# Optimization experiments

Hardware: AMD Instinct MI355X
Metric: run time of the kernel (lower is better)

The kernel has to match this reference:

```python
import jax, jax.numpy as jnp
import numpy as np

DELTA = 0.1  # init kwarg delta
EPS = 1e-12


def setup_inputs() -> dict:
    key = jax.random.key(0)
    k1, k2 = jax.random.split(key)
    N = 16384  # flattened element count; pairwise matrix is N x N (1 GB fp32)
    logits = jax.random.normal(k1, (N,), dtype=jnp.float32)
    targets = jax.random.randint(k2, (N,), 0, 2, dtype=jnp.int32)
    pos_weight = jnp.float32(1.0)  # registered buffer (non-trainable)
    return {"logits": logits, "targets": targets, "pos_weight": pos_weight}


def reference(logits, targets, pos_weight):
    y = targets.reshape(-1).astype(logits.dtype)
    x = logits.reshape(-1)
    pred = jax.nn.sigmoid(x)
    # g uses pred.detach() in torch -> stop_gradient here
    g = jnp.abs(jax.lax.stop_gradient(pred) - y)  # [N]
    n = g.shape[0]
    # brute-force O(n^2) gradient-density estimate (torch.no_grad block)
    diff = jnp.abs(g[:, None] - g[None, :])            # [N, N]
    GD = jnp.sum((diff <= DELTA).astype(g.dtype), axis=1) / DELTA  # [N]
    beta = jax.lax.stop_gradient(n / (GD + EPS))       # [N]
    # binary_cross_entropy_with_logits with pos_weight, reduction='none':
    # pw * y * softplus(-x) + (1 - y) * softplus(x)
    per_elem = pos_weight * y * jax.nn.softplus(-x) + (1.0 - y) * jax.nn.softplus(x)
    weighted = jnp.mean(beta * per_elem)
    pure_mean = jnp.mean(per_elem)
    return weighted, pure_mean
```

## Files before the change

kernel.cpp:

```cpp
#include <hip/hip_runtime.h>
#include <math.h>

#define GHM_DELTA 0.1f
#define GHM_EPS   1e-12f

__device__ __forceinline__ float softplus_ref(float x) {
    return fmaxf(x, 0.0f) + log1pf(expf(-fabsf(x)));
}

__device__ __forceinline__ float sigmoid_ref(float x) {
    return 1.0f / (1.0f + expf(-x));
}

__global__ __launch_bounds__(512) void ghm_fused(
    const float* __restrict__ logits,
    const int*   __restrict__ targets,
    const float* __restrict__ pos_weight,
    double*      __restrict__ partials,
    int n)
{
    __shared__ float gj[16384];
    __shared__ int   pc[16][32];

    const int tid = threadIdx.x;
    const int bx  = blockIdx.x;

    {
        const float4* l4 = reinterpret_cast<const float4*>(logits);
        const int4*   t4 = reinterpret_cast<const int4*>(targets);
        float4*       g4 = reinterpret_cast<float4*>(gj);
        const int nf4 = n >> 2;
        for (int k = tid; k < nf4; k += 512) {
            float4 x = l4[k];
            int4   y = t4[k];
            float4 r;
            r.x = fabsf(sigmoid_ref(x.x) - (float)y.x);
            r.y = fabsf(sigmoid_ref(x.y) - (float)y.y);
            r.z = fabsf(sigmoid_ref(x.z) - (float)y.z);
            r.w = fabsf(sigmoid_ref(x.w) - (float)y.w);
            g4[k] = r;
        }
    }
    __syncthreads();

    const int ilane = tid & 31;
    const int jpart = tid >> 5;
    const int ig    = bx * 32 + ilane;
    const float gi  = gj[ig];

    int c0 = 0, c1 = 0, c2 = 0, c3 = 0;
    const float4* lj = reinterpret_cast<const float4*>(gj) + jpart * 256;
    #pragma unroll 8
    for (int jj = 0; jj < 256; ++jj) {
        float4 v = lj[jj];
        c0 += (fabsf(gi - v.x) <= GHM_DELTA) ? 1 : 0;
        c1 += (fabsf(gi - v.y) <= GHM_DELTA) ? 1 : 0;
        c2 += (fabsf(gi - v.z) <= GHM_DELTA) ? 1 : 0;
        c3 += (fabsf(gi - v.w) <= GHM_DELTA) ? 1 : 0;
    }
    pc[jpart][ilane] = (c0 + c1) + (c2 + c3);
    __syncthreads();

    if (tid < 64) {
        double wd = 0.0, pd = 0.0;
        if (tid < 32) {
            int cnt = 0;
            #pragma unroll
            for (int p = 0; p < 16; ++p) cnt += pc[p][tid];
            const int i = bx * 32 + tid;
            float x  = logits[i];
            float y  = (float)targets[i];
            float GD   = (float)cnt / GHM_DELTA;
            float beta = (float)n / (GD + GHM_EPS);
            float pw   = pos_weight[0];
            float per  = pw * y * softplus_ref(-x) + (1.0f - y) * softplus_ref(x);
            wd = (double)(beta * per);
            pd = (double)per;
        }
        #pragma unroll
        for (int off = 32; off >= 1; off >>= 1) {
            wd += __shfl_down(wd, off, 64);
            pd += __shfl_down(pd, off, 64);
        }
        if (tid == 0) {
            partials[bx * 2]     = wd;
            partials[bx * 2 + 1] = pd;
        }
    }
}

__global__ __launch_bounds__(512) void ghm_reduce(
    const double* __restrict__ partials,
    float* __restrict__ out,
    int nb, int n)
{
    __shared__ double red[16];
    const int t = threadIdx.x;
    double wd = 0.0, pd = 0.0;
    for (int k = t; k < nb; k += 512) {
        wd += partials[2 * k];
        pd += partials[2 * k + 1];
    }
    #pragma unroll
    for (int off = 32; off >= 1; off >>= 1) {
        wd += __shfl_down(wd, off, 64);
        pd += __shfl_down(pd, off, 64);
    }
    const int wave = t >> 6;
    if ((t & 63) == 0) { red[wave * 2] = wd; red[wave * 2 + 1] = pd; }
    __syncthreads();
    if (t == 0) {
        double sw = 0.0, sp = 0.0;
        for (int k = 0; k < 8; ++k) { sw += red[2 * k]; sp += red[2 * k + 1]; }
        out[0] = (float)(sw / (double)n);
        out[1] = (float)(sp / (double)n);
    }
}

extern "C" void kernel_launch(void* const* d_in, const int* in_sizes, int n_in,
                              void* d_out, int out_size, void* d_ws, size_t ws_size,
                              hipStream_t stream) {
    const float* logits     = (const float*)d_in[0];
    const int*   targets    = (const int*)d_in[1];
    const float* pos_weight = (const float*)d_in[2];
    float* out = (float*)d_out;
    const int n = in_sizes[0];

    const int nb = n / 32;
    double* partials = (double*)d_ws;

    ghm_fused<<<nb, 512, 0, stream>>>(logits, targets, pos_weight, partials, n);
    ghm_reduce<<<1, 512, 0, stream>>>(partials, out, nb, n);
}
```

Before: 37.78 us.

## Register-block 8 rows per thread and widen blocks to 1024 threads

Each wave now holds 8 query values in registers and streams a strided quarter of the shared g array, so each LDS float4 load feeds 32 comparisons instead of 4. Per-row counts are reduced with wave shuffles and then summed over the four j-slices. Blocks grow to 1024 threads and the problem size is hardcoded to 16384, which removes the tail loop in the final reduce. The cost is more register pressure and a kernel that only handles N=16384.

```diff
diff --git a/kernel.cpp b/kernel.cpp
--- a/kernel.cpp
+++ b/kernel.cpp
@@ -3,34 +3,39 @@
 
 #define GHM_DELTA 0.1f
 #define GHM_EPS   1e-12f
+#define N_FIX     16384
+#define NBLK      512
+#define TI        32
+#define NTHR      1024
 
 __device__ __forceinline__ float softplus_ref(float x) {
     return fmaxf(x, 0.0f) + log1pf(expf(-fabsf(x)));
 }
-
 __device__ __forceinline__ float sigmoid_ref(float x) {
     return 1.0f / (1.0f + expf(-x));
 }
 
-__global__ __launch_bounds__(512) void ghm_fused(
+__global__ __launch_bounds__(1024, 8) void ghm_fused(
     const float* __restrict__ logits,
     const int*   __restrict__ targets,
     const float* __restrict__ pos_weight,
-    double*      __restrict__ partials,
-    int n)
+    double*      __restrict__ bpart)
 {
-    __shared__ float gj[16384];
-    __shared__ int   pc[16][32];
+    __shared__ float gj[N_FIX];
 
-    const int tid = threadIdx.x;
-    const int bx  = blockIdx.x;
+    const int tid  = threadIdx.x;
+    const int bx   = blockIdx.x;
+    const int lane = tid & 63;
+    const int wid  = tid >> 6;
+    const int ig   = wid & 3;
+    const int js   = wid >> 2;
 
     {
         const float4* l4 = reinterpret_cast<const float4*>(logits);
         const int4*   t4 = reinterpret_cast<const int4*>(targets);
         float4*       g4 = reinterpret_cast<float4*>(gj);
-        const int nf4 = n >> 2;
-        for (int k = tid; k < nf4; k += 512) {
+        #pragma unroll
+        for (int k = tid; k < N_FIX / 4; k += NTHR) {
             float4 x = l4[k];
             int4   y = t4[k];
             float4 r;
@@ -41,37 +46,78 @@
             g4[k] = r;
         }
     }
+
+    const int i0 = bx * TI + ig * 8;
+    float gi[8];
+    {
+        const float4* lx = reinterpret_cast<const float4*>(logits + i0);
+        const int4*   ty = reinterpret_cast<const int4*>(targets + i0);
+        float4 x0 = lx[0], x1 = lx[1];
+        int4   y0 = ty[0], y1 = ty[1];
+        gi[0] = fabsf(sigmoid_ref(x0.x) - (float)y0.x);
+        gi[1] = fabsf(sigmoid_ref(x0.y) - (float)y0.y);
+        gi[2] = fabsf(sigmoid_ref(x0.z) - (float)y0.z);
+        gi[3] = fabsf(sigmoid_ref(x0.w) - (float)y0.w);
+        gi[4] = fabsf(sigmoid_ref(x1.x) - (float)y1.x);
+        gi[5] = fabsf(sigmoid_ref(x1.y) - (float)y1.y);
+        gi[6] = fabsf(sigmoid_ref(x1.z) - (float)y1.z);
+        gi[7] = fabsf(sigmoid_ref(x1.w) - (float)y1.w);
+    }
     __syncthreads();
 
-    const int ilane = tid & 31;
-    const int jpart = tid >> 5;
-    const int ig    = bx * 32 + ilane;
-    const float gi  = gj[ig];
+    int c0 = 0, c1 = 0, c2 = 0, c3 = 0, c4 = 0, c5 = 0, c6 = 0, c7 = 0;
+    const float4* base = reinterpret_cast<const float4*>(gj) + js * 1024 + lane;
+    #pragma unroll 4
+    for (int jj = 0; jj < 16; ++jj) {
+        float4 v = base[(size_t)jj * 64];
+        c0 += (fabsf(gi[0] - v.x) <= GHM_DELTA) + (fabsf(gi[0] - v.y) <= GHM_DELTA)
+            + (fabsf(gi[0] - v.z) <= GHM_DELTA) + (fabsf(gi[0] - v.w) <= GHM_DELTA);
+        c1 += (fabsf(gi[1] - v.x) <= GHM_DELTA) + (fabsf(gi[1] - v.y) <= GHM_DELTA)
+            + (fabsf(gi[1] - v.z) <= GHM_DELTA) + (fabsf(gi[1] - v.w) <= GHM_DELTA);
+        c2 += (fabsf(gi[2] - v.x) <= GHM_DELTA) + (fabsf(gi[2] - v.y) <= GHM_DELTA)
+            + (fabsf(gi[2] - v.z) <= GHM_DELTA) + (fabsf(gi[2] - v.w) <= GHM_DELTA);
+        c3 += (fabsf(gi[3] - v.x) <= GHM_DELTA) + (fabsf(gi[3] - v.y) <= GHM_DELTA)
+            + (fabsf(gi[3] - v.z) <= GHM_DELTA) + (fabsf(gi[3] - v.w) <= GHM_DELTA);
+        c4 += (fabsf(gi[4] - v.x) <= GHM_DELTA) + (fabsf(gi[4] - v.y) <= GHM_DELTA)
+            + (fabsf(gi[4] - v.z) <= GHM_DELTA) + (fabsf(gi[4] - v.w) <= GHM_DELTA);
+        c5 += (fabsf(gi[5] - v.x) <= GHM_DELTA) + (fabsf(gi[5] - v.y) <= GHM_DELTA)
+            + (fabsf(gi[5] - v.z) <= GHM_DELTA) + (fabsf(gi[5] - v.w) <= GHM_DELTA);
+        c6 += (fabsf(gi[6] - v.x) <= GHM_DELTA) + (fabsf(gi[6] - v.y) <= GHM_DELTA)
+            + (fabsf(gi[6] - v.z) <= GHM_DELTA) + (fabsf(gi[6] - v.w) <= GHM_DELTA);
+        c7 += (fabsf(gi[7] - v.x) <= GHM_DELTA) + (fabsf(gi[7] - v.y) <= GHM_DELTA)
+            + (fabsf(gi[7] - v.z) <= GHM_DELTA) + (fabsf(gi[7] - v.w) <= GHM_DELTA);
+    }
 
-    int c0 = 0, c1 = 0, c2 = 0, c3 = 0;
-    const float4* lj = reinterpret_cast<const float4*>(gj) + jpart * 256;
-    #pragma unroll 8
-    for (int jj = 0; jj < 256; ++jj) {
-        float4 v = lj[jj];
-        c0 += (fabsf(gi - v.x) <= GHM_DELTA) ? 1 : 0;
-        c1 += (fabsf(gi - v.y) <= GHM_DELTA) ? 1 : 0;
-        c2 += (fabsf(gi - v.z) <= GHM_DELTA) ? 1 : 0;
-        c3 += (fabsf(gi - v.w) <= GHM_DELTA) ? 1 : 0;
+    #pragma unroll
+    for (int mask = 1; mask < 64; mask <<= 1) {
+        c0 += __shfl_xor(c0, mask, 64);
+        c1 += __shfl_xor(c1, mask, 64);
+        c2 += __shfl_xor(c2, mask, 64);
+        c3 += __shfl_xor(c3, mask, 64);
+        c4 += __shfl_xor(c4, mask, 64);
+        c5 += __shfl_xor(c5, mask, 64);
+        c6 += __shfl_xor(c6, mask, 64);
+        c7 += __shfl_xor(c7, mask, 64);
     }
-    pc[jpart][ilane] = (c0 + c1) + (c2 + c3);
+
+    __syncthreads();
+    int* pc = reinterpret_cast<int*>(gj);
+    if (lane == 0) {
+        int* d = pc + js * TI + ig * 8;
+        d[0] = c0; d[1] = c1; d[2] = c2; d[3] = c3;
+        d[4] = c4; d[5] = c5; d[6] = c6; d[7] = c7;
+    }
     __syncthreads();
 
     if (tid < 64) {
         double wd = 0.0, pd = 0.0;
-        if (tid < 32) {
-            int cnt = 0;
-            #pragma unroll
-            for (int p = 0; p < 16; ++p) cnt += pc[p][tid];
-            const int i = bx * 32 + tid;
+        if (tid < TI) {
+            int cnt = pc[tid] + pc[TI + tid] + pc[2 * TI + tid] + pc[3 * TI + tid];
+            const int i = bx * TI + tid;
             float x  = logits[i];
             float y  = (float)targets[i];
             float GD   = (float)cnt / GHM_DELTA;
-            float beta = (float)n / (GD + GHM_EPS);
+            float beta = (float)N_FIX / (GD + GHM_EPS);
             float pw   = pos_weight[0];
             float per  = pw * y * softplus_ref(-x) + (1.0f - y) * softplus_ref(x);
             wd = (double)(beta * per);
@@ -83,24 +129,19 @@
             pd += __shfl_down(pd, off, 64);
         }
         if (tid == 0) {
-            partials[bx * 2]     = wd;
-            partials[bx * 2 + 1] = pd;
+            bpart[bx * 2]     = wd;
+            bpart[bx * 2 + 1] = pd;
         }
     }
 }
 
 __global__ __launch_bounds__(512) void ghm_reduce(
-    const double* __restrict__ partials,
-    float* __restrict__ out,
-    int nb, int n)
+    const double* __restrict__ bpart, float* __restrict__ out, int n)
 {
     __shared__ double red[16];
     const int t = threadIdx.x;
-    double wd = 0.0, pd = 0.0;
-    for (int k = t; k < nb; k += 512) {
-        wd += partials[2 * k];
-        pd += partials[2 * k + 1];
-    }
+    double wd = bpart[2 * t];
+    double pd = bpart[2 * t + 1];
     #pragma unroll
     for (int off = 32; off >= 1; off >>= 1) {
         wd += __shfl_down(wd, off, 64);
@@ -111,6 +152,7 @@
     __syncthreads();
     if (t == 0) {
         double sw = 0.0, sp = 0.0;
+        #pragma unroll
         for (int k = 0; k < 8; ++k) { sw += red[2 * k]; sp += red[2 * k + 1]; }
         out[0] = (float)(sw / (double)n);
         out[1] = (float)(sp / (double)n);
@@ -126,9 +168,8 @@
     float* out = (float*)d_out;
     const int n = in_sizes[0];
 
-    const int nb = n / 32;
-    double* partials = (double*)d_ws;
+    double* bpart = (double*)d_ws;
 
-    ghm_fused<<<nb, 512, 0, stream>>>(logits, targets, pos_weight, partials, n);
-    ghm_reduce<<<1, 512, 0, stream>>>(partials, out, nb, n);
+    ghm_fused<<<NBLK, NTHR, 0, stream>>>(logits, targets, pos_weight, bpart);
+    ghm_reduce<<<1, NBLK, 0, stream>>>(bpart, out, n);
 }
```

Result: no change. 37.25 us (-1.4%).
